# Performance work log

Measured on AMD Instinct MI355X. Metric: run time of the kernel, lower is better.

The kernel has to match this reference:

```python
import jax, jax.numpy as jnp
import numpy as np

C = 512
CQK = C // 8   # 64
CV = C // 4    # 128

def setup_inputs() -> dict:
    key = jax.random.key(0)
    ks = jax.random.split(key, 10)
    B, H, W = 4, 64, 64
    s = 1.0 / np.sqrt(C)
    x = jax.random.normal(ks[0], (B, C, H, W), dtype=jnp.float32)
    Wq = jax.random.normal(ks[1], (CQK, C), dtype=jnp.float32) * s
    bq = jnp.zeros((CQK,), jnp.float32)
    Wk = jax.random.normal(ks[2], (CQK, C), dtype=jnp.float32) * s
    bk = jnp.zeros((CQK,), jnp.float32)
    Wv = jax.random.normal(ks[3], (CV, C), dtype=jnp.float32) * s
    bv = jnp.zeros((CV,), jnp.float32)
    Wo = jax.random.normal(ks[4], (C, CV), dtype=jnp.float32) * (1.0 / np.sqrt(CV))
    bo = jnp.zeros((C,), jnp.float32)
    gamma = jnp.ones((1,), jnp.float32) * 0.5  # nonzero so out path matters
    return {"x": x, "Wq": Wq, "bq": bq, "Wk": Wk, "bk": bk,
            "Wv": Wv, "bv": bv, "Wo": Wo, "bo": bo, "gamma": gamma}

def reference(x, Wq, bq, Wk, bk, Wv, bv, Wo, bo, gamma):
    B, C_, H, W = x.shape
    N = H * W
    xf = x.reshape(B, C_, N)                       # [B,C,N]
    # 1x1 convs == channel matmuls
    q = jnp.einsum('oc,bcn->bno', Wq, xf) + bq     # [B,N,Cqk]
    k = jnp.einsum('oc,bcn->bon', Wk, xf) + bk[None, :, None]  # [B,Cqk,N]
    v = jnp.einsum('oc,bcn->bon', Wv, xf) + bv[None, :, None]  # [B,Cv,N]
    attn = jax.nn.softmax(jnp.einsum('bno,bom->bnm', q, k), axis=-1)  # [B,N,N]
    out = jnp.einsum('bom,bnm->bon', v, attn)      # [B,Cv,N]
    out = jnp.einsum('oc,bcn->bon', Wo, out) + bo[None, :, None]  # [B,C,N]
    out = out.reshape(B, C_, H, W)
    return x + gamma * out
```

## Files before the change

kernel.cpp:

```cpp
#include <hip/hip_runtime.h>
#include <cstdint>
#include <cstddef>

#define N_SP 4096
#define C_IN 512
#define C_QK 64
#define C_V  128
#define LOG2E 1.4426950408889634f

typedef unsigned short u16;
typedef __attribute__((ext_vector_type(8))) short bf16x8;
typedef __attribute__((ext_vector_type(4))) float f32x4;
typedef __attribute__((ext_vector_type(16))) float f32x16;

__device__ __forceinline__ u16 f2bf(float f) {
    union { float f; uint32_t u; } x; x.f = f;
    const uint32_t r = x.u + 0x7fffu + ((x.u >> 16) & 1u);
    return (u16)(r >> 16);
}
__device__ __forceinline__ float bf2f(u16 b) {
    union { uint32_t u; float f; } x; x.u = ((uint32_t)b) << 16;
    return x.f;
}

__device__ __forceinline__ void* swzPtr(const void* base, int row, int colByte) {
    return (char*)base + row * 128 + (colByte ^ ((row & 7) << 4));
}

__global__ __launch_bounds__(256) void wconv_kernel(
    const float* __restrict__ Wq, const float* __restrict__ Wk,
    const float* __restrict__ Wv, const float* __restrict__ Wo,
    u16* __restrict__ Wqb, u16* __restrict__ Wkb,
    u16* __restrict__ Wvb, u16* __restrict__ Wob)
{
    const int i = (blockIdx.x << 8) + threadIdx.x;
    const float* src; u16* dst; int off;
    if (i < 8192)       { src = Wq; dst = Wqb; off = i; }
    else if (i < 16384) { src = Wk; dst = Wkb; off = i - 8192; }
    else if (i < 32768) { src = Wv; dst = Wvb; off = i - 16384; }
    else                { src = Wo; dst = Wob; off = i - 32768; }
    const float4 v = *(const float4*)(src + ((size_t)off << 2));
    ushort4 h;
    h.x = f2bf(v.x); h.y = f2bf(v.y); h.z = f2bf(v.z); h.w = f2bf(v.w);
    *(ushort4*)(dst + ((size_t)off << 2)) = h;
}

__global__ __launch_bounds__(256) void transpose_kernel(
    const float* __restrict__ x, u16* __restrict__ xb)
{
    __shared__ u16 ts[64 * 64];
    const int t = threadIdx.x;
    const int b  = blockIdx.x & 3;
    const int cc = (blockIdx.x >> 2) & 7;
    const int nc = blockIdx.x >> 5;
    const int c0 = cc << 6, n0 = nc << 6;
    const float* xs = x + ((size_t)(b * C_IN + c0) << 12) + n0;
    for (int u = t; u < 1024; u += 256) {
        const int c = u >> 4, nq = (u & 15) << 2;
        const float4 v = *(const float4*)(xs + ((size_t)c << 12) + nq);
        ushort4 h;
        h.x = f2bf(v.x); h.y = f2bf(v.y); h.z = f2bf(v.z); h.w = f2bf(v.w);
        *(ushort4*)((char*)ts + c * 128 + ((nq << 1) ^ (((c >> 3) & 7) << 4))) = h;
    }
    __syncthreads();
    for (int u = t; u < 512; u += 256) {
        const int n = u >> 3, cg = u & 7;
        u16 pk[8];
        #pragma unroll
        for (int j = 0; j < 8; ++j) {
            const int c = (cg << 3) + j;
            pk[j] = *(const u16*)((char*)ts + c * 128 + ((n << 1) ^ (cg << 4)));
        }
        *(ushort4*)(xb + ((size_t)((b << 12) + n0 + n) << 9) + c0 + (cg << 3)) =
            *(ushort4*)&pk[0];
        *(ushort4*)(xb + ((size_t)((b << 12) + n0 + n) << 9) + c0 + (cg << 3) + 4) =
            *(ushort4*)&pk[4];
    }
}

__global__ __launch_bounds__(256) void qkv_kernel(
    const u16* __restrict__ xb,
    const u16* __restrict__ Wqb, const float* __restrict__ bq,
    const u16* __restrict__ Wkb, const float* __restrict__ bk,
    const u16* __restrict__ Wvb, const float* __restrict__ bv,
    u16* __restrict__ Qb, u16* __restrict__ Kf, u16* __restrict__ Vf)
{
    __shared__ u16 wt[64 * 64];
    __shared__ u16 xt[64 * 64];
    const int t = threadIdx.x;
    const int l = t & 63, w = t >> 6;
    const int lo = l & 15, hi = l >> 4;
    const int b  = blockIdx.x & 3;
    const int ot = (blockIdx.x >> 2) & 3;
    const int n0 = (blockIdx.x >> 4) << 6;
    const u16* Wbase = (ot == 0) ? Wqb : (ot == 1) ? Wkb : (Wvb + ((ot - 2) << 6) * C_IN);
    f32x4 acc[4];
    #pragma unroll
    for (int ti = 0; ti < 4; ++ti) acc[ti] = (f32x4){0.f, 0.f, 0.f, 0.f};

    for (int cc = 0; cc < 8; ++cc) {
        const int c0 = cc << 6;
        for (int u = t; u < 512; u += 256) {
            const int i = u >> 3, cb = (u & 7) << 4;
            *(uint4*)swzPtr(wt, i, cb) =
                *(const uint4*)(Wbase + (size_t)i * C_IN + c0 + (cb >> 1));
        }
        for (int u = t; u < 512; u += 256) {
            const int i = u >> 3, cb = (u & 7) << 4;
            *(uint4*)swzPtr(xt, i, cb) =
                *(const uint4*)(xb + ((size_t)((b << 12) + n0 + i) << 9) + c0 + (cb >> 1));
        }
        __syncthreads();
        if (ot < 2) {
            const bf16x8 af0 = *(const bf16x8*)swzPtr(xt, (w << 4) + lo, hi << 4);
            const bf16x8 af1 = *(const bf16x8*)swzPtr(xt, (w << 4) + lo, 64 + (hi << 4));
            #pragma unroll
            for (int ti = 0; ti < 4; ++ti) {
                const bf16x8 bf0 = *(const bf16x8*)swzPtr(wt, (ti << 4) + lo, hi << 4);
                const bf16x8 bf1 = *(const bf16x8*)swzPtr(wt, (ti << 4) + lo, 64 + (hi << 4));
                acc[ti] = __builtin_amdgcn_mfma_f32_16x16x32_bf16(af0, bf0, acc[ti], 0, 0, 0);
                acc[ti] = __builtin_amdgcn_mfma_f32_16x16x32_bf16(af1, bf1, acc[ti], 0, 0, 0);
            }
        } else {
            const bf16x8 af0 = *(const bf16x8*)swzPtr(wt, (w << 4) + lo, hi << 4);
            const bf16x8 af1 = *(const bf16x8*)swzPtr(wt, (w << 4) + lo, 64 + (hi << 4));
            #pragma unroll
            for (int ti = 0; ti < 4; ++ti) {
                const bf16x8 bf0 = *(const bf16x8*)swzPtr(xt, (ti << 4) + lo, hi << 4);
                const bf16x8 bf1 = *(const bf16x8*)swzPtr(xt, (ti << 4) + lo, 64 + (hi << 4));
                acc[ti] = __builtin_amdgcn_mfma_f32_16x16x32_bf16(af0, bf0, acc[ti], 0, 0, 0);
                acc[ti] = __builtin_amdgcn_mfma_f32_16x16x32_bf16(af1, bf1, acc[ti], 0, 0, 0);
            }
        }
        __syncthreads();
    }
    const int kt = n0 >> 6;
    if (ot == 0) {
        #pragma unroll
        for (int ti = 0; ti < 4; ++ti) {
            const float bias = bq[(ti << 4) + lo];
            #pragma unroll
            for (int r = 0; r < 4; ++r) {
                const int nrow = (w << 4) + (hi << 2) + r;
                Qb[((size_t)((b << 12) + n0 + nrow) << 6) + (ti << 4) + lo] =
                    f2bf((acc[ti][r] + bias) * LOG2E);
            }
        }
    } else if (ot == 1) {
        #pragma unroll
        for (int ti = 0; ti < 4; ++ti) {
            const int ch = (ti << 4) + lo;
            const float bias = bk[ch];
            #pragma unroll
            for (int r = 0; r < 4; ++r) {
                const int key = (w << 4) + (hi << 2) + r;
                const int sid = (ti << 1) + (key >> 5);
                const int lpos = (((ch >> 3) & 1) << 5) + (key & 31);
                Kf[(((size_t)((b << 6) + kt) << 3) + sid) * 512 + (lpos << 3) + (ch & 7)] =
                    f2bf(acc[ti][r] + bias);
            }
        }
    } else {
        #pragma unroll
        for (int r = 0; r < 4; ++r) {
            const int cv = ((ot - 2) << 6) + (w << 4) + (hi << 2) + r;
            const float bias = bv[cv];
            #pragma unroll
            for (int ti = 0; ti < 4; ++ti) {
                const int nl = (ti << 4) + lo;
                const int sv = ((cv >> 5) << 2) + ti;
                const int lpos = (((nl >> 3) & 1) << 5) + (cv & 31);
                Vf[(((size_t)((b << 6) + kt) << 4) + sv) * 512 + (lpos << 3) + (nl & 7)] =
                    f2bf(acc[ti][r] + bias);
            }
        }
    }
}


#define KLOAD(dst, ktl)                                                        \
    {                                                                          \
        const size_t o_ = ((size_t)(((s << 4) + ((ktl) & 15)) << 3)) * 512;    \
        _Pragma("unroll")                                                      \
        for (int i_ = 0; i_ < 8; ++i_)                                         \
            dst[i_] = *(const bf16x8*)(kfb + o_ + i_ * 512);                   \
    }

#define VLOAD(dst, ktl, tjIdx)                                                 \
    {                                                                          \
        const size_t o_ = ((size_t)(((s << 4) + (ktl)) << 4) + ((tjIdx) << 2)) * 512; \
        _Pragma("unroll")                                                      \
        for (int i_ = 0; i_ < 4; ++i_)                                         \
            dst[i_] = *(const bf16x8*)(vfb + o_ + i_ * 512);                   \
    }

#define TILE(kt, kfU, kfP)                                                    \
    {                                                                         \
        bf16x8 vA[4], vB[4], vC[4];                                           \
        VLOAD(vA, kt, 0);                     \
        f32x16 sa0, sa1;                                                      \
        _Pragma("unroll")                                                     \
        for (int i = 0; i < 16; ++i) { sa0[i] = 0.f; sa1[i] = 0.f; }          \
        __builtin_amdgcn_s_setprio(1);                                        \
        _Pragma("unroll")                                                     \
        for (int ks = 0; ks < 4; ++ks) {                                      \
            sa0 = __builtin_amdgcn_mfma_f32_32x32x16_bf16(kfU[(ks << 1)], qf[ks], sa0, 0, 0, 0);     \
            sa1 = __builtin_amdgcn_mfma_f32_32x32x16_bf16(kfU[(ks << 1) + 1], qf[ks], sa1, 0, 0, 0); \
        }                                                                     \
        __builtin_amdgcn_s_setprio(0);                                        \
        KLOAD(kfP, (kt) + 1);                           \
        VLOAD(vB, kt, 1);                                 \
        float p0[16], p1[16];                                                 \
        _Pragma("unroll")                                                     \
        for (int i = 0; i < 16; ++i) {                                        \
            p0[i] = exp2f(sa0[i]);                                            \
            p1[i] = exp2f(sa1[i]);                                            \
        }                                                                     \
        float sm8[8];                                                         \
        _Pragma("unroll")                                                     \
        for (int i = 0; i < 8; ++i) sm8[i] = (p0[i] + p0[i + 8]) + (p1[i] + p1[i + 8]); \
        _Pragma("unroll")                                                     \
        for (int i = 0; i < 4; ++i) sm8[i] += sm8[i + 4];                     \
        lsum += (sm8[0] + sm8[1]) + (sm8[2] + sm8[3]);                        \
        VLOAD(vC, kt, 2);                                 \
        uint32_t P2[2][4][2];                                                 \
        _Pragma("unroll")                                                     \
        for (int g = 0; g < 4; ++g) {                                         \
            _Pragma("unroll")                                                 \
            for (int pr = 0; pr < 2; ++pr) {                                  \
                asm("v_cvt_pk_bf16_f32 %0, %1, %2"                            \
                    : "=v"(P2[0][g][pr]) : "v"(p0[4 * g + 2 * pr]), "v"(p0[4 * g + 2 * pr + 1])); \
                asm("v_cvt_pk_bf16_f32 %0, %1, %2"                            \
                    : "=v"(P2[1][g][pr]) : "v"(p1[4 * g + 2 * pr]), "v"(p1[4 * g + 2 * pr + 1])); \
            }                                                                 \
        }                                                                     \
        bf16x8 pf[4];                                                         \
        _Pragma("unroll")                                                     \
        for (int ks = 0; ks < 4; ++ks) {                                      \
            const int iE = ks << 1, iO = iE + 1;                              \
            uint32_t fr[4];                                                   \
            _Pragma("unroll")                                                 \
            for (int pr = 0; pr < 2; ++pr) {                                  \
                const uint32_t X = P2[iE >> 2][iE & 3][pr];                   \
                const uint32_t Y = P2[iO >> 2][iO & 3][pr];                   \
                const uint32_t send = h ? X : Y;                              \
                const uint32_t recv = (uint32_t)__shfl_xor((int)send, 32);    \
                fr[pr]     = h ? recv : X;                                    \
                fr[2 + pr] = h ? Y : recv;                                    \
            }                                                                 \
            pf[ks] = *(bf16x8*)fr;                                            \
        }                                                                     \
        __builtin_amdgcn_s_setprio(1);                                        \
        _Pragma("unroll")                                                     \
        for (int ks = 0; ks < 4; ++ks)                                        \
            oacc[0] = __builtin_amdgcn_mfma_f32_32x32x16_bf16(vA[ks], pf[ks], oacc[0], 0, 0, 0); \
        __builtin_amdgcn_s_setprio(0);                                        \
        VLOAD(vA, kt, 3);                                 \
        __builtin_amdgcn_s_setprio(1);                                        \
        _Pragma("unroll")                                                     \
        for (int ks = 0; ks < 4; ++ks)                                        \
            oacc[1] = __builtin_amdgcn_mfma_f32_32x32x16_bf16(vB[ks], pf[ks], oacc[1], 0, 0, 0); \
        _Pragma("unroll")                                                     \
        for (int ks = 0; ks < 4; ++ks)                                        \
            oacc[2] = __builtin_amdgcn_mfma_f32_32x32x16_bf16(vC[ks], pf[ks], oacc[2], 0, 0, 0); \
        _Pragma("unroll")                                                     \
        for (int ks = 0; ks < 4; ++ks)                                        \
            oacc[3] = __builtin_amdgcn_mfma_f32_32x32x16_bf16(vA[ks], pf[ks], oacc[3], 0, 0, 0); \
        __builtin_amdgcn_s_setprio(0);                                        \
    }

__global__ __launch_bounds__(256, 2) void attn_kernel(
    const u16* __restrict__ Qb, const u16* __restrict__ Kf,
    const u16* __restrict__ Vf, u16* __restrict__ po,
    float* __restrict__ pl)
{
    const int t = threadIdx.x;
    const int l = t & 63, w = t >> 6;
    const int l31 = l & 31, h = l >> 5;
    const int b = blockIdx.x & 3;
    const int s = (blockIdx.x >> 2) & 3;
    const int qc = blockIdx.x >> 4;
    const int n0 = qc << 7;

    const u16* qp = Qb + ((size_t)((b << 12) + n0 + (w << 5) + l31) << 6) + (h << 3);
    bf16x8 qf[4];
    #pragma unroll
    for (int ks = 0; ks < 4; ++ks) qf[ks] = *(const bf16x8*)(qp + (ks << 4));

    const u16* kfb = Kf + (((size_t)(b << 6)) << 12) + (l << 3);
    const u16* vfb = Vf + (((size_t)(b << 6)) << 13) + (l << 3);

    float lsum = 0.f;
    f32x16 oacc[4];
    #pragma unroll
    for (int tj = 0; tj < 4; ++tj)
        #pragma unroll
        for (int i = 0; i < 16; ++i) oacc[tj][i] = 0.f;

    bf16x8 kfA[8], kfB[8];
    KLOAD(kfA, 0);

    for (int kt2 = 0; kt2 < 16; kt2 += 2) {
        TILE(kt2, kfA, kfB);
        TILE(kt2 + 1, kfB, kfA);
    }

    lsum += __shfl_xor(lsum, 32);
    u16* pod = po + ((size_t)blockIdx.x << 14);
    #pragma unroll
    for (int tj = 0; tj < 4; ++tj)
        #pragma unroll
        for (int r = 0; r < 16; ++r) {
            const int cv = (tj << 5) + (r & 3) + ((r >> 2) << 3) + (h << 2);
            pod[(cv << 7) + (w << 5) + l31] = f2bf(oacc[tj][r]);
        }
    if (h == 0) pl[(blockIdx.x << 7) + (w << 5) + l31] = lsum;
}

__global__ __launch_bounds__(256) void combine_kernel(
    const u16* __restrict__ po, const float* __restrict__ pl,
    u16* __restrict__ Ob)
{
    __shared__ float invl[128];
    __shared__ float tr[64][132];
    const int t = threadIdx.x;
    const int b = blockIdx.x & 3;
    const int qc = blockIdx.x >> 2;
    int slot[4];
    #pragma unroll
    for (int s = 0; s < 4; ++s) slot[s] = b + (s << 2) + (qc << 4);
    if (t < 128) {
        float lg = 0.f;
        #pragma unroll
        for (int s = 0; s < 4; ++s) lg += pl[(slot[s] << 7) + t];
        invl[t] = 1.0f / lg;
    }
    __syncthreads();
    #pragma unroll
    for (int qh = 0; qh < 2; ++qh) {
        for (int u = t; u < 2048; u += 256) {
            const int cv = u >> 4, q4 = (u & 15) << 2;
            const int q = (qh << 6) + q4;
            float a0 = 0.f, a1 = 0.f, a2 = 0.f, a3 = 0.f;
            #pragma unroll
            for (int s = 0; s < 4; ++s) {
                const ushort4 hv =
                    *(const ushort4*)(po + ((size_t)slot[s] << 14) + (cv << 7) + q);
                a0 += bf2f(hv.x); a1 += bf2f(hv.y);
                a2 += bf2f(hv.z); a3 += bf2f(hv.w);
            }
            tr[q4 + 0][cv] = a0 * invl[q];
            tr[q4 + 1][cv] = a1 * invl[q + 1];
            tr[q4 + 2][cv] = a2 * invl[q + 2];
            tr[q4 + 3][cv] = a3 * invl[q + 3];
        }
        __syncthreads();
        for (int u = t; u < 2048; u += 256) {
            const int q = u >> 5, c4 = (u & 31) << 2;
            const float4 v = *(const float4*)&tr[q][c4];
            ushort4 o;
            o.x = f2bf(v.x); o.y = f2bf(v.y); o.z = f2bf(v.z); o.w = f2bf(v.w);
            const int n = (qc << 7) + (qh << 6) + q;
            *(ushort4*)(Ob + ((size_t)((b << 12) + n) << 7) + c4) = o;
        }
        __syncthreads();
    }
}

__global__ __launch_bounds__(256) void proj_kernel(
    const u16* __restrict__ Ob, const u16* __restrict__ Wob,
    const float* __restrict__ bo, const float* __restrict__ x,
    const float* __restrict__ gamma_p, float* __restrict__ out)
{
    __shared__ union {
        struct { u16 wl0[64 * 64]; u16 wl1[64 * 64]; u16 ob0[64 * 64]; u16 ob1[64 * 64]; } s;
        float tr[64 * 64];
    } sm;
    const int t = threadIdx.x;
    const int l = t & 63, w = t >> 6;
    const int lo = l & 15, hi = l >> 4;
    const int b  = blockIdx.x & 3;
    const int co0 = ((blockIdx.x >> 2) & 7) << 6;
    const int n0  = (blockIdx.x >> 5) << 6;
    for (int u = t; u < 1024; u += 256) {
        const int i = u >> 4, cb = (u & 15) << 4;
        *(uint4*)swzPtr((cb < 128) ? sm.s.wl0 : sm.s.wl1, i, cb & 127) =
            *(const uint4*)(Wob + (size_t)(co0 + i) * C_V + (cb >> 1));
    }
    for (int u = t; u < 1024; u += 256) {
        const int i = u >> 4, cb = (u & 15) << 4;
        *(uint4*)swzPtr((cb < 128) ? sm.s.ob0 : sm.s.ob1, i, cb & 127) =
            *(const uint4*)(Ob + ((size_t)((b << 12) + n0 + i) << 7) + (cb >> 1));
    }
    __syncthreads();
    const int arow = (w << 4) + lo;
    const bf16x8 af00 = *(const bf16x8*)swzPtr(sm.s.wl0, arow, hi << 4);
    const bf16x8 af01 = *(const bf16x8*)swzPtr(sm.s.wl0, arow, 64 + (hi << 4));
    const bf16x8 af10 = *(const bf16x8*)swzPtr(sm.s.wl1, arow, hi << 4);
    const bf16x8 af11 = *(const bf16x8*)swzPtr(sm.s.wl1, arow, 64 + (hi << 4));
    f32x4 acc[4];
    #pragma unroll
    for (int ti = 0; ti < 4; ++ti) {
        const int brow = (ti << 4) + lo;
        f32x4 z = (f32x4){0.f, 0.f, 0.f, 0.f};
        z = __builtin_amdgcn_mfma_f32_16x16x32_bf16(af00, *(const bf16x8*)swzPtr(sm.s.ob0, brow, hi << 4), z, 0, 0, 0);
        z = __builtin_amdgcn_mfma_f32_16x16x32_bf16(af01, *(const bf16x8*)swzPtr(sm.s.ob0, brow, 64 + (hi << 4)), z, 0, 0, 0);
        z = __builtin_amdgcn_mfma_f32_16x16x32_bf16(af10, *(const bf16x8*)swzPtr(sm.s.ob1, brow, hi << 4), z, 0, 0, 0);
        acc[ti] = __builtin_amdgcn_mfma_f32_16x16x32_bf16(af11, *(const bf16x8*)swzPtr(sm.s.ob1, brow, 64 + (hi << 4)), z, 0, 0, 0);
    }
    __syncthreads();
    #pragma unroll
    for (int ti = 0; ti < 4; ++ti)
        #pragma unroll
        for (int r = 0; r < 4; ++r) {
            const int co = (w << 4) + (hi << 2) + r;
            const int n  = (ti << 4) + lo;
            sm.tr[(co << 6) + (n ^ (((co >> 2) & 3) << 2))] = acc[ti][r];
        }
    __syncthreads();
    const float g = gamma_p[0];
    for (int u = t; u < 1024; u += 256) {
        const int co = u >> 4, n4 = (u & 15) << 2;
        const float4 av = *(const float4*)&sm.tr[(co << 6) + (n4 ^ (((co >> 2) & 3) << 2))];
        const int o = co0 + co;
        const size_t off = ((size_t)(b * C_IN + o) << 12) + n0 + n4;
        const float4 xv = *(const float4*)(x + off);
        const float bias = bo[o];
        float4 rs;
        rs.x = xv.x + g * (av.x + bias);
        rs.y = xv.y + g * (av.y + bias);
        rs.z = xv.z + g * (av.z + bias);
        rs.w = xv.w + g * (av.w + bias);
        *(float4*)(out + off) = rs;
    }
}

extern "C" void kernel_launch(void* const* d_in, const int* in_sizes, int n_in,
                              void* d_out, int out_size, void* d_ws, size_t ws_size,
                              hipStream_t stream) {
    (void)in_sizes; (void)n_in; (void)out_size; (void)ws_size;
    const float* x  = (const float*)d_in[0];
    const float* Wq = (const float*)d_in[1];
    const float* bq = (const float*)d_in[2];
    const float* Wk = (const float*)d_in[3];
    const float* bk = (const float*)d_in[4];
    const float* Wv = (const float*)d_in[5];
    const float* bv = (const float*)d_in[6];
    const float* Wo = (const float*)d_in[7];
    const float* bo = (const float*)d_in[8];
    const float* gm = (const float*)d_in[9];
    float* out = (float*)d_out;
    u16* xb = (u16*)d_ws;
    u16* po = (u16*)d_ws;
    u16* Qb = (u16*)((char*)d_ws + ((size_t)16 << 20));
    u16* Kf = Qb + (size_t)4 * N_SP * C_QK;
    u16* Vf = Kf + (size_t)4 * N_SP * C_QK;
    float* pl = (float*)((char*)d_ws + ((size_t)24 << 20));
    u16* Ob = (u16*)((char*)d_ws + ((size_t)24 << 20) + (256 << 10));
    u16* Wqb = (u16*)((char*)d_ws + ((size_t)24 << 20) + (256 << 10) + ((size_t)4 << 20));
    u16* Wkb = Wqb + 64 * 512;
    u16* Wvb = Wkb + 64 * 512;
    u16* Wob = Wvb + 128 * 512;
    wconv_kernel<<<192, 256, 0, stream>>>(Wq, Wk, Wv, Wo, Wqb, Wkb, Wvb, Wob);
    transpose_kernel<<<2048, 256, 0, stream>>>(x, xb);
    qkv_kernel<<<1024, 256, 0, stream>>>(xb, Wqb, bq, Wkb, bk, Wvb, bv, Qb, Kf, Vf);
    attn_kernel<<<512, 256, 0, stream>>>(Qb, Kf, Vf, po, pl);
    combine_kernel<<<128, 256, 0, stream>>>(po, pl, Ob);
    proj_kernel<<<2048, 256, 0, stream>>>(Ob, Wob, bo, x, gm, out);
}
```

Measured before the change: 106.4 us.

## Compute all QKV channels per block and use permlane32 swap in attention

```diff
diff --git a/kernel.cpp b/kernel.cpp
--- a/kernel.cpp
+++ b/kernel.cpp
@@ -85,25 +85,27 @@
     const u16* __restrict__ Wvb, const float* __restrict__ bv,
     u16* __restrict__ Qb, u16* __restrict__ Kf, u16* __restrict__ Vf)
 {
-    __shared__ u16 wt[64 * 64];
+    __shared__ u16 wt[256 * 64];
     __shared__ u16 xt[64 * 64];
     const int t = threadIdx.x;
     const int l = t & 63, w = t >> 6;
     const int lo = l & 15, hi = l >> 4;
     const int b  = blockIdx.x & 3;
-    const int ot = (blockIdx.x >> 2) & 3;
-    const int n0 = (blockIdx.x >> 4) << 6;
-    const u16* Wbase = (ot == 0) ? Wqb : (ot == 1) ? Wkb : (Wvb + ((ot - 2) << 6) * C_IN);
-    f32x4 acc[4];
-    #pragma unroll
-    for (int ti = 0; ti < 4; ++ti) acc[ti] = (f32x4){0.f, 0.f, 0.f, 0.f};
+    const int n0 = (blockIdx.x >> 2) << 6;
+    f32x4 acc[4][4];
+    #pragma unroll
+    for (int i = 0; i < 4; ++i)
+        #pragma unroll
+        for (int j = 0; j < 4; ++j) acc[i][j] = (f32x4){0.f, 0.f, 0.f, 0.f};
 
     for (int cc = 0; cc < 8; ++cc) {
         const int c0 = cc << 6;
-        for (int u = t; u < 512; u += 256) {
+        for (int u = t; u < 2048; u += 256) {
             const int i = u >> 3, cb = (u & 7) << 4;
-            *(uint4*)swzPtr(wt, i, cb) =
-                *(const uint4*)(Wbase + (size_t)i * C_IN + c0 + (cb >> 1));
+            const u16* src = (i < 64) ? (Wqb + (size_t)i * C_IN)
+                           : (i < 128) ? (Wkb + (size_t)(i - 64) * C_IN)
+                                       : (Wvb + (size_t)(i - 128) * C_IN);
+            *(uint4*)swzPtr(wt, i, cb) = *(const uint4*)(src + c0 + (cb >> 1));
         }
         for (int u = t; u < 512; u += 256) {
             const int i = u >> 3, cb = (u & 7) << 4;
@@ -111,69 +113,91 @@
                 *(const uint4*)(xb + ((size_t)((b << 12) + n0 + i) << 9) + c0 + (cb >> 1));
         }
         __syncthreads();
-        if (ot < 2) {
-            const bf16x8 af0 = *(const bf16x8*)swzPtr(xt, (w << 4) + lo, hi << 4);
-            const bf16x8 af1 = *(const bf16x8*)swzPtr(xt, (w << 4) + lo, 64 + (hi << 4));
-            #pragma unroll
-            for (int ti = 0; ti < 4; ++ti) {
-                const bf16x8 bf0 = *(const bf16x8*)swzPtr(wt, (ti << 4) + lo, hi << 4);
-                const bf16x8 bf1 = *(const bf16x8*)swzPtr(wt, (ti << 4) + lo, 64 + (hi << 4));
-                acc[ti] = __builtin_amdgcn_mfma_f32_16x16x32_bf16(af0, bf0, acc[ti], 0, 0, 0);
-                acc[ti] = __builtin_amdgcn_mfma_f32_16x16x32_bf16(af1, bf1, acc[ti], 0, 0, 0);
+        if (w < 2) {
+            bf16x8 af[4][2];
+            #pragma unroll
+            for (int tn = 0; tn < 4; ++tn) {
+                af[tn][0] = *(const bf16x8*)swzPtr(xt, (tn << 4) + lo, hi << 4);
+                af[tn][1] = *(const bf16x8*)swzPtr(xt, (tn << 4) + lo, 64 + (hi << 4));
+            }
+            #pragma unroll
+            for (int to = 0; to < 4; ++to) {
+                const int wr = (w << 6) + (to << 4) + lo;
+                const bf16x8 bf0 = *(const bf16x8*)swzPtr(wt, wr, hi << 4);
+                const bf16x8 bf1 = *(const bf16x8*)swzPtr(wt, wr, 64 + (hi << 4));
+                #pragma unroll
+                for (int tn = 0; tn < 4; ++tn) {
+                    acc[tn][to] = __builtin_amdgcn_mfma_f32_16x16x32_bf16(af[tn][0], bf0, acc[tn][to], 0, 0, 0);
+                    acc[tn][to] = __builtin_amdgcn_mfma_f32_16x16x32_bf16(af[tn][1], bf1, acc[tn][to], 0, 0, 0);
+                }
             }
         } else {
-            const bf16x8 af0 = *(const bf16x8*)swzPtr(wt, (w << 4) + lo, hi << 4);
-            const bf16x8 af1 = *(const bf16x8*)swzPtr(wt, (w << 4) + lo, 64 + (hi << 4));
-            #pragma unroll
-            for (int ti = 0; ti < 4; ++ti) {
-                const bf16x8 bf0 = *(const bf16x8*)swzPtr(xt, (ti << 4) + lo, hi << 4);
-                const bf16x8 bf1 = *(const bf16x8*)swzPtr(xt, (ti << 4) + lo, 64 + (hi << 4));
-                acc[ti] = __builtin_amdgcn_mfma_f32_16x16x32_bf16(af0, bf0, acc[ti], 0, 0, 0);
-                acc[ti] = __builtin_amdgcn_mfma_f32_16x16x32_bf16(af1, bf1, acc[ti], 0, 0, 0);
+            bf16x8 af[4][2];
+            #pragma unroll
+            for (int tc = 0; tc < 4; ++tc) {
+                const int wr = 128 + ((w - 2) << 6) + (tc << 4) + lo;
+                af[tc][0] = *(const bf16x8*)swzPtr(wt, wr, hi << 4);
+                af[tc][1] = *(const bf16x8*)swzPtr(wt, wr, 64 + (hi << 4));
+            }
+            #pragma unroll
+            for (int tn = 0; tn < 4; ++tn) {
+                const bf16x8 bf0 = *(const bf16x8*)swzPtr(xt, (tn << 4) + lo, hi << 4);
+                const bf16x8 bf1 = *(const bf16x8*)swzPtr(xt, (tn << 4) + lo, 64 + (hi << 4));
+                #pragma unroll
+                for (int tc = 0; tc < 4; ++tc) {
+                    acc[tc][tn] = __builtin_amdgcn_mfma_f32_16x16x32_bf16(af[tc][0], bf0, acc[tc][tn], 0, 0, 0);
+                    acc[tc][tn] = __builtin_amdgcn_mfma_f32_16x16x32_bf16(af[tc][1], bf1, acc[tc][tn], 0, 0, 0);
+                }
             }
         }
         __syncthreads();
     }
     const int kt = n0 >> 6;
-    if (ot == 0) {
-        #pragma unroll
-        for (int ti = 0; ti < 4; ++ti) {
-            const float bias = bq[(ti << 4) + lo];
+    if (w == 0) {
+        #pragma unroll
+        for (int to = 0; to < 4; ++to) {
+            const float bias = bq[(to << 4) + lo];
+            #pragma unroll
+            for (int tn = 0; tn < 4; ++tn)
+                #pragma unroll
+                for (int r = 0; r < 4; ++r) {
+                    const int nrow = (tn << 4) + (hi << 2) + r;
+                    Qb[((size_t)((b << 12) + n0 + nrow) << 6) + (to << 4) + lo] =
+                        f2bf((acc[tn][to][r] + bias) * LOG2E);
+                }
+        }
+    } else if (w == 1) {
+        #pragma unroll
+        for (int to = 0; to < 4; ++to) {
+            const int ch = (to << 4) + lo;
+            const float bias = bk[ch];
+            #pragma unroll
+            for (int tn = 0; tn < 4; ++tn)
+                #pragma unroll
+                for (int r = 0; r < 4; ++r) {
+                    const int key = (tn << 4) + (hi << 2) + r;
+                    const int sid = (to << 1) + (key >> 5);
+                    const int lpos = (((ch >> 3) & 1) << 5) + (key & 31);
+                    Kf[(((size_t)((b << 6) + kt) << 3) + sid) * 512 + (lpos << 3) + (ch & 7)] =
+                        f2bf(acc[tn][to][r] + bias);
+                }
+        }
+    } else {
+        #pragma unroll
+        for (int tc = 0; tc < 4; ++tc)
             #pragma unroll
             for (int r = 0; r < 4; ++r) {
-                const int nrow = (w << 4) + (hi << 2) + r;
-                Qb[((size_t)((b << 12) + n0 + nrow) << 6) + (ti << 4) + lo] =
-                    f2bf((acc[ti][r] + bias) * LOG2E);
-            }
-        }
-    } else if (ot == 1) {
-        #pragma unroll
-        for (int ti = 0; ti < 4; ++ti) {
-            const int ch = (ti << 4) + lo;
-            const float bias = bk[ch];
-            #pragma unroll
-            for (int r = 0; r < 4; ++r) {
-                const int key = (w << 4) + (hi << 2) + r;
-                const int sid = (ti << 1) + (key >> 5);
-                const int lpos = (((ch >> 3) & 1) << 5) + (key & 31);
-                Kf[(((size_t)((b << 6) + kt) << 3) + sid) * 512 + (lpos << 3) + (ch & 7)] =
-                    f2bf(acc[ti][r] + bias);
-            }
-        }
-    } else {
-        #pragma unroll
-        for (int r = 0; r < 4; ++r) {
-            const int cv = ((ot - 2) << 6) + (w << 4) + (hi << 2) + r;
-            const float bias = bv[cv];
-            #pragma unroll
-            for (int ti = 0; ti < 4; ++ti) {
-                const int nl = (ti << 4) + lo;
-                const int sv = ((cv >> 5) << 2) + ti;
-                const int lpos = (((nl >> 3) & 1) << 5) + (cv & 31);
-                Vf[(((size_t)((b << 6) + kt) << 4) + sv) * 512 + (lpos << 3) + (nl & 7)] =
-                    f2bf(acc[ti][r] + bias);
-            }
-        }
+                const int cv = ((w - 2) << 6) + (tc << 4) + (hi << 2) + r;
+                const float bias = bv[cv];
+                #pragma unroll
+                for (int tn = 0; tn < 4; ++tn) {
+                    const int nl = (tn << 4) + lo;
+                    const int sv = ((cv >> 5) << 2) + tn;
+                    const int lpos = (((nl >> 3) & 1) << 5) + (cv & 31);
+                    Vf[(((size_t)((b << 6) + kt) << 4) + sv) * 512 + (lpos << 3) + (nl & 7)] =
+                        f2bf(acc[tc][tn][r] + bias);
+                }
+            }
     }
 }
 
@@ -197,7 +221,7 @@
 #define TILE(kt, kfU, kfP)                                                    \
     {                                                                         \
         bf16x8 vA[4], vB[4], vC[4];                                           \
-        VLOAD(vA, kt, 0);                     \
+        VLOAD(vA, kt, 0);                                                     \
         f32x16 sa0, sa1;                                                      \
         _Pragma("unroll")                                                     \
         for (int i = 0; i < 16; ++i) { sa0[i] = 0.f; sa1[i] = 0.f; }          \
@@ -208,8 +232,8 @@
             sa1 = __builtin_amdgcn_mfma_f32_32x32x16_bf16(kfU[(ks << 1) + 1], qf[ks], sa1, 0, 0, 0); \
         }                                                                     \
         __builtin_amdgcn_s_setprio(0);                                        \
-        KLOAD(kfP, (kt) + 1);                           \
-        VLOAD(vB, kt, 1);                                 \
+        KLOAD(kfP, (kt) + 1);                                                 \
+        VLOAD(vB, kt, 1);                                                     \
         float p0[16], p1[16];                                                 \
         _Pragma("unroll")                                                     \
         for (int i = 0; i < 16; ++i) {                                        \
@@ -222,7 +246,7 @@
         _Pragma("unroll")                                                     \
         for (int i = 0; i < 4; ++i) sm8[i] += sm8[i + 4];                     \
         lsum += (sm8[0] + sm8[1]) + (sm8[2] + sm8[3]);                        \
-        VLOAD(vC, kt, 2);                                 \
+        VLOAD(vC, kt, 2);                                                     \
         uint32_t P2[2][4][2];                                                 \
         _Pragma("unroll")                                                     \
         for (int g = 0; g < 4; ++g) {                                         \
@@ -241,12 +265,11 @@
             uint32_t fr[4];                                                   \
             _Pragma("unroll")                                                 \
             for (int pr = 0; pr < 2; ++pr) {                                  \
-                const uint32_t X = P2[iE >> 2][iE & 3][pr];                   \
-                const uint32_t Y = P2[iO >> 2][iO & 3][pr];                   \
-                const uint32_t send = h ? X : Y;                              \
-                const uint32_t recv = (uint32_t)__shfl_xor((int)send, 32);    \
-                fr[pr]     = h ? recv : X;                                    \
-                fr[2 + pr] = h ? Y : recv;                                    \
+                uint32_t X = P2[iE >> 2][iE & 3][pr];                         \
+                uint32_t Y = P2[iO >> 2][iO & 3][pr];                         \
+                asm("v_permlane32_swap_b32 %0, %1" : "+v"(X), "+v"(Y));       \
+                fr[pr]     = X;                            \
+                fr[2 + pr] = Y;                            \
             }                                                                 \
             pf[ks] = *(bf16x8*)fr;                                            \
         }                                                                     \
@@ -255,7 +278,7 @@
         for (int ks = 0; ks < 4; ++ks)                                        \
             oacc[0] = __builtin_amdgcn_mfma_f32_32x32x16_bf16(vA[ks], pf[ks], oacc[0], 0, 0, 0); \
         __builtin_amdgcn_s_setprio(0);                                        \
-        VLOAD(vA, kt, 3);                                 \
+        VLOAD(vA, kt, 3);                                                     \
         __builtin_amdgcn_s_setprio(1);                                        \
         _Pragma("unroll")                                                     \
         for (int ks = 0; ks < 4; ++ks)                                        \
@@ -463,7 +486,7 @@
     u16* Wob = Wvb + 128 * 512;
     wconv_kernel<<<192, 256, 0, stream>>>(Wq, Wk, Wv, Wo, Wqb, Wkb, Wvb, Wob);
     transpose_kernel<<<2048, 256, 0, stream>>>(x, xb);
-    qkv_kernel<<<1024, 256, 0, stream>>>(xb, Wqb, bq, Wkb, bk, Wvb, bv, Qb, Kf, Vf);
+    qkv_kernel<<<256, 256, 0, stream>>>(xb, Wqb, bq, Wkb, bk, Wvb, bv, Qb, Kf, Vf);
     attn_kernel<<<512, 256, 0, stream>>>(Qb, Kf, Vf, po, pl);
     combine_kernel<<<128, 256, 0, stream>>>(po, pl, Ob);
     proj_kernel<<<2048, 256, 0, stream>>>(Ob, Wob, bo, x, gm, out);
```

After: 118.3 us. +11.2%, slower.
